# Performance work log

Hardware: AMD Instinct MI355X
Metric: run time of the kernel (lower is better)

## Reference

```python
import jax, jax.numpy as jnp
import numpy as np

K = 3          # kernel size
PAD = 1        # padding
# deformable conv v2: offset conv (2*K*K ch), modulator conv (K*K ch, 2*sigmoid), main 3x3 conv, ReLU


def _conv2d(x, w, b):
    y = jax.lax.conv_general_dilated(x, w, (1, 1), ((PAD, PAD), (PAD, PAD)),
                                     dimension_numbers=('NCHW', 'OIHW', 'NCHW'))
    return y + b[None, :, None, None]


def _bilinear_gather(x, py, px):
    # x: [B,C,H,W]; py/px: [B,K2,H,W] float sample coords; zero outside image.
    B, C, H, W = x.shape
    y0 = jnp.floor(py)
    x0 = jnp.floor(px)
    wy1 = py - y0
    wx1 = px - x0
    wy0 = 1.0 - wy1
    wx0 = 1.0 - wx1
    xf = x.reshape(B, C, H * W)

    def gather(yi, xi):
        valid = (yi >= 0) & (yi <= H - 1) & (xi >= 0) & (xi <= W - 1)
        yc = jnp.clip(yi, 0, H - 1).astype(jnp.int32)
        xc = jnp.clip(xi, 0, W - 1).astype(jnp.int32)
        idx = (yc * W + xc).reshape(B, -1)                      # [B, K2*H*W]
        v = jax.vmap(lambda xb, ib: xb[:, ib])(xf, idx)         # [B, C, K2*H*W]
        v = v.reshape(B, C, *yi.shape[1:])                      # [B, C, K2, H, W]
        return v * valid[:, None].astype(x.dtype)

    return (gather(y0, x0) * (wy0 * wx0)[:, None]
            + gather(y0, x0 + 1) * (wy0 * wx1)[:, None]
            + gather(y0 + 1, x0) * (wy1 * wx0)[:, None]
            + gather(y0 + 1, x0 + 1) * (wy1 * wx1)[:, None])


def _deform_conv(data, w, b, w_off, b_off, w_mod, b_mod):
    B, Cin, H, W = data.shape
    off = _conv2d(data, w_off, b_off)                           # [B, 2*K2, H, W]
    mask = 2.0 * jax.nn.sigmoid(_conv2d(data, w_mod, b_mod))    # [B, K2, H, W]
    off = off.reshape(B, K * K, 2, H, W)                        # (dy, dx) per tap
    dy, dx = off[:, :, 0], off[:, :, 1]
    ki, kj = jnp.meshgrid(jnp.arange(K), jnp.arange(K), indexing='ij')
    ki = ki.reshape(-1).astype(data.dtype)
    kj = kj.reshape(-1).astype(data.dtype)
    hs = jnp.arange(H, dtype=data.dtype)
    ws = jnp.arange(W, dtype=data.dtype)
    py = hs[None, None, :, None] - PAD + ki[None, :, None, None] + dy
    px = ws[None, None, None, :] - PAD + kj[None, :, None, None] + dx
    sampled = _bilinear_gather(data, py, px)                    # [B, Cin, K2, H, W]
    sampled = sampled * mask[:, None]
    out = jnp.einsum('bckhw,ock->bohw', sampled, w.reshape(w.shape[0], Cin, K * K))
    return out + b[None, :, None, None]


def setup_inputs() -> dict:
    key = jax.random.key(0)
    ks = jax.random.split(key, 7)
    B, Cin, Cout, H, W = 8, 64, 64, 128, 128
    fan = Cin * K * K
    return {
        'data': jax.random.normal(ks[0], (B, Cin, H, W), jnp.float32),
        'w': jax.random.normal(ks[1], (Cout, Cin, K, K), jnp.float32) / np.sqrt(fan),
        'b': jax.random.normal(ks[2], (Cout,), jnp.float32) * 0.01,
        'w_off': jax.random.normal(ks[3], (2 * K * K, Cin, K, K), jnp.float32) * (0.1 / np.sqrt(fan)),
        'b_off': jnp.zeros((2 * K * K,), jnp.float32),
        'w_mod': jax.random.normal(ks[4], (K * K, Cin, K, K), jnp.float32) * (0.1 / np.sqrt(fan)),
        'b_mod': jnp.zeros((K * K,), jnp.float32),
    }


def reference(data, w, b, w_off, b_off, w_mod, b_mod):
    return jax.nn.relu(_deform_conv(data, w, b, w_off, b_off, w_mod, b_mod))
```

## Files before the change

kernel.cpp:

```cpp
#include <hip/hip_runtime.h>
#include <hip/hip_fp16.h>
#include <cstdint>


typedef _Float16 half8 __attribute__((ext_vector_type(8)));
typedef __attribute__((ext_vector_type(4))) float floatx4;

__device__ __forceinline__ unsigned int pack2h(float lo, float hi) {
    __half2 h = __floats2half2_rn(lo, hi);
    union { __half2 h; unsigned int u; } cv; cv.h = h;
    return cv.u;
}
__device__ __forceinline__ unsigned int blend2h(unsigned int a, unsigned int b,
                                                unsigned int c, unsigned int d,
                                                const __half2* w) {
    union { unsigned int u; __half2 h; } A, B, C, D, O;
    A.u = a; B.u = b; C.u = c; D.u = d;
    __half2 s = __hmul2(A.h, w[0]);
    s = __hfma2(B.h, w[1], s);
    s = __hfma2(C.h, w[2], s);
    s = __hfma2(D.h, w[3], s);
    O.h = s;
    return O.u;
}

#define OFF_DATAT 0u
#define OFF_OFFP  16777216u
#define OFF_WM    30932992u
#define OFF_W27   31006720u
#define OFF_B27   31043584u

__global__ __launch_bounds__(256) void prep_k(const float* __restrict__ x,
                                              unsigned short* __restrict__ xt,
                                              const float* __restrict__ w,
                                              const float* __restrict__ w_off,
                                              const float* __restrict__ w_mod,
                                              const float* __restrict__ b_off,
                                              const float* __restrict__ b_mod,
                                              unsigned short* __restrict__ wpackM,
                                              unsigned short* __restrict__ wq,
                                              float* __restrict__ bias27) {
    __shared__ float tile[64][65];
    int blk = blockIdx.x;
    if (blk < 2048) {
        int b    = blk >> 8;
        int pos0 = (blk & 255) << 6;
        int lane = threadIdx.x & 63;
        int g    = threadIdx.x >> 6;
        for (int c = g; c < 64; c += 4)
            tile[c][lane] = x[(((b << 6) + c) << 14) + pos0 + lane];
        __syncthreads();
        int c2 = lane & 31;
        for (int i = g; i < 32; i += 4) {
            int pr = (i << 1) + (lane >> 5);
            unsigned int d = pack2h(tile[c2 << 1][pr], tile[(c2 << 1) + 1][pr]);
            *(unsigned int*)&xt[((size_t)((b << 14) + pos0 + pr) << 6) + (c2 << 1)] = d;
        }
        return;
    }
    int t = (blk - 2048) * 256 + threadIdx.x;
    if (t < 64 * 576) {
        int o = t / 576, kk = t % 576;
        int k = kk >> 6, c = kk & 63;
        wpackM[t] = __half_as_ushort(__float2half_rn(w[(o * 64 + c) * 9 + k]));
        return;
    }
    t -= 64 * 576;
    if (t < 32 * 576) {
        int o = t / 576, kk = t % 576;
        int k = kk >> 6, c = kk & 63;
        float v = 0.f;
        if (o < 18)      v = w_off[(o * 64 + c) * 9 + k];
        else if (o < 27) v = w_mod[((o - 18) * 64 + c) * 9 + k];
        int s = o >> 4, r = o & 15;
        int chh = c >> 5, q = (c >> 3) & 3, j = c & 7;
        int dst = (((((k << 1) + chh) << 1) + s) << 9) + (q << 7) + (r << 3) + j;
        wq[dst] = __half_as_ushort(__float2half_rn(v));
        if (kk == 0) bias27[o] = (o < 18) ? b_off[o] : (o < 27 ? b_mod[o - 18] : 0.f);
    }
}

__global__ __launch_bounds__(256) void conv27_k(const unsigned short* __restrict__ xt,
                                                const unsigned short* __restrict__ wq,
                                                const float* __restrict__ bias27,
                                                float* __restrict__ offP) {
    int blk   = blockIdx.x;
    int b     = blk >> 7;
    int patch = blk & 127;
    int m     = patch >> 1;
    int h     = patch & 1;
    int tid   = threadIdx.x;
    int lane  = tid & 63, wv = tid >> 6;
    int r = lane & 15, q = lane >> 4;

    const unsigned short* xb = xt + ((size_t)b << 20);
    int rb  = (m << 1) - 1;
    int cxb = (h << 6) + (wv << 4) + r - 1;
    int chq = (q << 3);

    floatx4 acc[4] = {};
    #pragma unroll
    for (int k = 0; k < 9; ++k) {
        int ki = k / 3, kj = k % 3;
        #pragma unroll
        for (int chh = 0; chh < 2; ++chh) {
            int abase = ((((k << 1) + chh) << 1) << 9) + (lane << 3);
            half8 a0 = *(const half8*)&wq[abase];
            half8 a1 = *(const half8*)&wq[abase + 512];
            #pragma unroll
            for (int tr = 0; tr < 2; ++tr) {
                int sy = rb + tr + ki;
                int sx = cxb + kj;
                half8 bf = {};
                if ((unsigned)sy < 128u && (unsigned)sx < 128u)
                    bf = *(const half8*)&xb[(size_t)(((sy << 7) + sx) << 6) + (chh << 5) + chq];
                acc[0 + tr] = __builtin_amdgcn_mfma_f32_16x16x32_f16(a0, bf, acc[0 + tr], 0, 0, 0);
                acc[2 + tr] = __builtin_amdgcn_mfma_f32_16x16x32_f16(a1, bf, acc[2 + tr], 0, 0, 0);
            }
        }
    }

    #pragma unroll
    for (int s = 0; s < 2; ++s) {
        #pragma unroll
        for (int tr = 0; tr < 2; ++tr) {
            #pragma unroll
            for (int reg = 0; reg < 4; ++reg) {
                int oc = (s << 4) + (q << 2) + reg;
                if (oc >= 27) continue;
                int pos = (((m << 1) + tr) << 7) + (h << 6) + (wv << 4) + r;
                float v = acc[(s << 1) + tr][reg] + bias27[oc];
                int kk, comp;
                if (oc < 18) { kk = oc >> 1; comp = oc & 1; }
                else         { kk = oc - 18; comp = 2; v = 2.f / (1.f + __expf(-v)); }
                offP[(size_t)(((b * 9 + kk) * 3 + comp) << 14) + pos] = v;
            }
        }
    }
}

__global__ __launch_bounds__(256, 3) void deform_main_k(const unsigned short* __restrict__ xt,
                                                        const unsigned short* __restrict__ wpackM,
                                                        const float* __restrict__ offP,
                                                        const float* __restrict__ bias,
                                                        float* __restrict__ out) {
    __shared__ ushort4 pOff[576];
    __shared__ uint4   pW[576];
    __shared__ unsigned short samp[2][64][72];
    int blk  = blockIdx.x;
    int b    = blk >> 8;
    int pos0 = (blk & 255) << 6;
    int tid  = threadIdx.x;
    int lane = tid & 63, wv = tid >> 6;
    int r = lane & 15, q = lane >> 4;
    int pg = lane >> 3;
    int j8 = lane & 7;

    const char* xbb = (const char*)(xt + ((size_t)b << 20));

    for (int e = tid; e < 576; e += 256) {
        int k = e >> 6, p = e & 63;
        int pos = pos0 + p;
        const float* offk = offP + ((size_t)((b * 9 + k) * 3) << 14);
        float dy = offk[pos];
        float dx = offk[16384 + pos];
        float m  = offk[32768 + pos];
        float py = (float)(pos >> 7) + (float)(k / 3 - 1) + dy;
        float px = (float)(pos & 127) + (float)(k % 3 - 1) + dx;
        float y0f = floorf(py), x0f = floorf(px);
        int y0 = (int)y0f, x0 = (int)x0f;
        float wy1 = py - y0f, wx1 = px - x0f;
        float wy0 = 1.f - wy1, wx0 = 1.f - wx1;
        bool vy0 = (y0 >= 0) && (y0 < 128);
        bool vy1 = (y0 >= -1) && (y0 < 127);
        bool vx0 = (x0 >= 0) && (x0 < 128);
        bool vx1 = (x0 >= -1) && (x0 < 127);
        float w00 = (vy0 && vx0) ? m * wy0 * wx0 : 0.f;
        float w01 = (vy0 && vx1) ? m * wy0 * wx1 : 0.f;
        float w10 = (vy1 && vx0) ? m * wy1 * wx0 : 0.f;
        float w11 = (vy1 && vx1) ? m * wy1 * wx1 : 0.f;
        int y0c = min(max(y0, 0), 127), y1c = min(max(y0 + 1, 0), 127);
        int x0c = min(max(x0, 0), 127), x1c = min(max(x0 + 1, 0), 127);
        ushort4 io;
        io.x = (unsigned short)((y0c << 7) + x0c);
        io.y = (unsigned short)((y0c << 7) + x1c);
        io.z = (unsigned short)((y1c << 7) + x0c);
        io.w = (unsigned short)((y1c << 7) + x1c);
        pOff[e] = io;
        union { uint4 u; __half2 h[4]; } pw;
        pw.h[0] = __float2half2_rn(w00);
        pw.h[1] = __float2half2_rn(w01);
        pw.h[2] = __float2half2_rn(w10);
        pw.h[3] = __float2half2_rn(w11);
        pW[e] = pw.u;
    }
    __syncthreads();

    floatx4 acc[4] = {};
    const char* xp = xbb + (j8 << 4);
    const unsigned short* wrow = wpackM + ((wv << 4) + r) * 576 + (q << 3);

    uint4   c00[2][2], c01[2][2], c10[2][2], c11[2][2];
    uint4   cwS[2][2];
    ushort4 nio[2];
    uint4   ncw[2];
    half8   afC[2], afN[2];

    auto readParams = [&](int k) {
        #pragma unroll
        for (int i = 0; i < 2; ++i) {
            int e  = (k << 6) + (wv << 4) + (i << 3) + pg;
            nio[i] = pOff[e];
            ncw[i] = pW[e];
        }
    };
    auto issueInto = [&](int s) {
        #pragma unroll
        for (int i = 0; i < 2; ++i) {
            cwS[s][i] = ncw[i];
            c00[s][i] = *(const uint4*)(xp + ((int)nio[i].x << 7));
            c01[s][i] = *(const uint4*)(xp + ((int)nio[i].y << 7));
            c10[s][i] = *(const uint4*)(xp + ((int)nio[i].z << 7));
            c11[s][i] = *(const uint4*)(xp + ((int)nio[i].w << 7));
        }
    };
    auto blendStore = [&](int s, int buf) {
        #pragma unroll
        for (int i = 0; i < 2; ++i) {
            int p = (wv << 4) + (i << 3) + pg;
            union { uint4 u; __half2 h[4]; } W; W.u = cwS[s][i];
            uint4 o4;
            o4.x = blend2h(c00[s][i].x, c01[s][i].x, c10[s][i].x, c11[s][i].x, W.h);
            o4.y = blend2h(c00[s][i].y, c01[s][i].y, c10[s][i].y, c11[s][i].y, W.h);
            o4.z = blend2h(c00[s][i].z, c01[s][i].z, c10[s][i].z, c11[s][i].z, W.h);
            o4.w = blend2h(c00[s][i].w, c01[s][i].w, c10[s][i].w, c11[s][i].w, W.h);
            *(uint4*)&samp[buf][p][j8 << 3] = o4;
        }
    };

    auto ldsBarrier = [&]() {
        asm volatile("s_waitcnt lgkmcnt(0)\n\ts_barrier" ::: "memory");
    };

    readParams(0); issueInto(0);
    readParams(1); issueInto(1);
    afC[0] = *(const half8*)&wrow[0];
    afC[1] = *(const half8*)&wrow[32];
    blendStore(0, 0);
    readParams(2);

    #pragma unroll
    for (int k = 0; k < 9; ++k) {
        if (k <= 6) issueInto(k & 1);
        if (k < 8) {
            afN[0] = *(const half8*)&wrow[((k + 1) << 6)];
            afN[1] = *(const half8*)&wrow[((k + 1) << 6) + 32];
        }
        ldsBarrier();
        #pragma unroll
        for (int ch = 0; ch < 2; ++ch) {
            #pragma unroll
            for (int nt = 0; nt < 4; ++nt) {
                half8 bfrag = *(const half8*)&samp[k & 1][(nt << 4) + r][(ch << 5) + (q << 3)];
                acc[nt] = __builtin_amdgcn_mfma_f32_16x16x32_f16(afC[ch], bfrag, acc[nt], 0, 0, 0);
            }
        }
        if (k < 8) {
            blendStore((k + 1) & 1, (k + 1) & 1);
            if (k <= 5) readParams(k + 3);
            afC[0] = afN[0];
            afC[1] = afN[1];
        }
    }

    #pragma unroll
    for (int nt = 0; nt < 4; ++nt) {
        #pragma unroll
        for (int reg = 0; reg < 4; ++reg) {
            int oc  = (wv << 4) + (q << 2) + reg;
            int pos = pos0 + (nt << 4) + r;
            float v = acc[nt][reg] + bias[oc];
            out[(size_t)(((b << 6) + oc) << 14) + pos] = fmaxf(v, 0.f);
        }
    }
}

extern "C" void kernel_launch(void* const* d_in, const int* in_sizes, int n_in,
                              void* d_out, int out_size, void* d_ws, size_t ws_size,
                              hipStream_t stream) {
    const float* data  = (const float*)d_in[0];
    const float* w     = (const float*)d_in[1];
    const float* bias  = (const float*)d_in[2];
    const float* w_off = (const float*)d_in[3];
    const float* b_off = (const float*)d_in[4];
    const float* w_mod = (const float*)d_in[5];
    const float* b_mod = (const float*)d_in[6];
    float* out = (float*)d_out;

    char* ws = (char*)d_ws;
    unsigned short* dataT   = (unsigned short*)(ws + OFF_DATAT);
    float*          offP    = (float*)(ws + OFF_OFFP);
    unsigned short* wpackM  = (unsigned short*)(ws + OFF_WM);
    unsigned short* wq      = (unsigned short*)(ws + OFF_W27);
    float*          bias27  = (float*)(ws + OFF_B27);

    prep_k<<<2264, 256, 0, stream>>>(data, dataT, w, w_off, w_mod,
                                     b_off, b_mod, wpackM, wq, bias27);
    conv27_k<<<1024, 256, 0, stream>>>(dataT, wq, bias27, offP);
    deform_main_k<<<2048, 256, 0, stream>>>(dataT, wpackM, offP, bias, out);
}
```

Measured before the change: 160.7 us.

## Fuse three kernels into one cooperative persistent kernel with grid syncs

```diff
diff --git a/kernel.cpp b/kernel.cpp
--- a/kernel.cpp
+++ b/kernel.cpp
@@ -1,6 +1,9 @@
 #include <hip/hip_runtime.h>
 #include <hip/hip_fp16.h>
+#include <hip/hip_cooperative_groups.h>
 #include <cstdint>
+
+namespace cg = cooperative_groups;
 
 
 typedef _Float16 half8 __attribute__((ext_vector_type(8)));
@@ -30,257 +33,260 @@
 #define OFF_W27   31006720u
 #define OFF_B27   31043584u
 
-__global__ __launch_bounds__(256) void prep_k(const float* __restrict__ x,
-                                              unsigned short* __restrict__ xt,
-                                              const float* __restrict__ w,
-                                              const float* __restrict__ w_off,
-                                              const float* __restrict__ w_mod,
-                                              const float* __restrict__ b_off,
-                                              const float* __restrict__ b_mod,
-                                              unsigned short* __restrict__ wpackM,
-                                              unsigned short* __restrict__ wq,
-                                              float* __restrict__ bias27) {
-    __shared__ float tile[64][65];
-    int blk = blockIdx.x;
-    if (blk < 2048) {
-        int b    = blk >> 8;
-        int pos0 = (blk & 255) << 6;
-        int lane = threadIdx.x & 63;
-        int g    = threadIdx.x >> 6;
-        for (int c = g; c < 64; c += 4)
-            tile[c][lane] = x[(((b << 6) + c) << 14) + pos0 + lane];
-        __syncthreads();
-        int c2 = lane & 31;
-        for (int i = g; i < 32; i += 4) {
-            int pr = (i << 1) + (lane >> 5);
-            unsigned int d = pack2h(tile[c2 << 1][pr], tile[(c2 << 1) + 1][pr]);
-            *(unsigned int*)&xt[((size_t)((b << 14) + pos0 + pr) << 6) + (c2 << 1)] = d;
-        }
-        return;
-    }
-    int t = (blk - 2048) * 256 + threadIdx.x;
-    if (t < 64 * 576) {
-        int o = t / 576, kk = t % 576;
-        int k = kk >> 6, c = kk & 63;
-        wpackM[t] = __half_as_ushort(__float2half_rn(w[(o * 64 + c) * 9 + k]));
-        return;
-    }
-    t -= 64 * 576;
-    if (t < 32 * 576) {
-        int o = t / 576, kk = t % 576;
-        int k = kk >> 6, c = kk & 63;
-        float v = 0.f;
-        if (o < 18)      v = w_off[(o * 64 + c) * 9 + k];
-        else if (o < 27) v = w_mod[((o - 18) * 64 + c) * 9 + k];
-        int s = o >> 4, r = o & 15;
-        int chh = c >> 5, q = (c >> 3) & 3, j = c & 7;
-        int dst = (((((k << 1) + chh) << 1) + s) << 9) + (q << 7) + (r << 3) + j;
-        wq[dst] = __half_as_ushort(__float2half_rn(v));
-        if (kk == 0) bias27[o] = (o < 18) ? b_off[o] : (o < 27 ? b_mod[o - 18] : 0.f);
-    }
-}
-
-__global__ __launch_bounds__(256) void conv27_k(const unsigned short* __restrict__ xt,
-                                                const unsigned short* __restrict__ wq,
-                                                const float* __restrict__ bias27,
-                                                float* __restrict__ offP) {
-    int blk   = blockIdx.x;
-    int b     = blk >> 7;
-    int patch = blk & 127;
-    int m     = patch >> 1;
-    int h     = patch & 1;
-    int tid   = threadIdx.x;
-    int lane  = tid & 63, wv = tid >> 6;
-    int r = lane & 15, q = lane >> 4;
-
-    const unsigned short* xb = xt + ((size_t)b << 20);
-    int rb  = (m << 1) - 1;
-    int cxb = (h << 6) + (wv << 4) + r - 1;
-    int chq = (q << 3);
-
-    floatx4 acc[4] = {};
-    #pragma unroll
-    for (int k = 0; k < 9; ++k) {
-        int ki = k / 3, kj = k % 3;
-        #pragma unroll
-        for (int chh = 0; chh < 2; ++chh) {
-            int abase = ((((k << 1) + chh) << 1) << 9) + (lane << 3);
-            half8 a0 = *(const half8*)&wq[abase];
-            half8 a1 = *(const half8*)&wq[abase + 512];
-            #pragma unroll
-            for (int tr = 0; tr < 2; ++tr) {
-                int sy = rb + tr + ki;
-                int sx = cxb + kj;
-                half8 bf = {};
-                if ((unsigned)sy < 128u && (unsigned)sx < 128u)
-                    bf = *(const half8*)&xb[(size_t)(((sy << 7) + sx) << 6) + (chh << 5) + chq];
-                acc[0 + tr] = __builtin_amdgcn_mfma_f32_16x16x32_f16(a0, bf, acc[0 + tr], 0, 0, 0);
-                acc[2 + tr] = __builtin_amdgcn_mfma_f32_16x16x32_f16(a1, bf, acc[2 + tr], 0, 0, 0);
-            }
-        }
-    }
-
-    #pragma unroll
-    for (int s = 0; s < 2; ++s) {
-        #pragma unroll
-        for (int tr = 0; tr < 2; ++tr) {
-            #pragma unroll
-            for (int reg = 0; reg < 4; ++reg) {
-                int oc = (s << 4) + (q << 2) + reg;
-                if (oc >= 27) continue;
-                int pos = (((m << 1) + tr) << 7) + (h << 6) + (wv << 4) + r;
-                float v = acc[(s << 1) + tr][reg] + bias27[oc];
-                int kk, comp;
-                if (oc < 18) { kk = oc >> 1; comp = oc & 1; }
-                else         { kk = oc - 18; comp = 2; v = 2.f / (1.f + __expf(-v)); }
-                offP[(size_t)(((b * 9 + kk) * 3 + comp) << 14) + pos] = v;
-            }
-        }
-    }
-}
-
-__global__ __launch_bounds__(256, 3) void deform_main_k(const unsigned short* __restrict__ xt,
-                                                        const unsigned short* __restrict__ wpackM,
-                                                        const float* __restrict__ offP,
-                                                        const float* __restrict__ bias,
-                                                        float* __restrict__ out) {
-    __shared__ ushort4 pOff[576];
-    __shared__ uint4   pW[576];
-    __shared__ unsigned short samp[2][64][72];
-    int blk  = blockIdx.x;
-    int b    = blk >> 8;
-    int pos0 = (blk & 255) << 6;
+__global__ __launch_bounds__(256, 4) void mega_k(const float* __restrict__ x,
+                                                 unsigned short* __restrict__ xt,
+                                                 const float* __restrict__ w,
+                                                 const float* __restrict__ w_off,
+                                                 const float* __restrict__ w_mod,
+                                                 const float* __restrict__ b_off,
+                                                 const float* __restrict__ b_mod,
+                                                 unsigned short* __restrict__ wpackM,
+                                                 unsigned short* __restrict__ wq,
+                                                 float* __restrict__ bias27,
+                                                 float* __restrict__ offP,
+                                                 const float* __restrict__ bias,
+                                                 float* __restrict__ out) {
+    __shared__ __align__(16) char smem[32256];
+    cg::grid_group grid = cg::this_grid();
+
     int tid  = threadIdx.x;
     int lane = tid & 63, wv = tid >> 6;
     int r = lane & 15, q = lane >> 4;
-    int pg = lane >> 3;
-    int j8 = lane & 7;
-
-    const char* xbb = (const char*)(xt + ((size_t)b << 20));
-
-    for (int e = tid; e < 576; e += 256) {
-        int k = e >> 6, p = e & 63;
-        int pos = pos0 + p;
-        const float* offk = offP + ((size_t)((b * 9 + k) * 3) << 14);
-        float dy = offk[pos];
-        float dx = offk[16384 + pos];
-        float m  = offk[32768 + pos];
-        float py = (float)(pos >> 7) + (float)(k / 3 - 1) + dy;
-        float px = (float)(pos & 127) + (float)(k % 3 - 1) + dx;
-        float y0f = floorf(py), x0f = floorf(px);
-        int y0 = (int)y0f, x0 = (int)x0f;
-        float wy1 = py - y0f, wx1 = px - x0f;
-        float wy0 = 1.f - wy1, wx0 = 1.f - wx1;
-        bool vy0 = (y0 >= 0) && (y0 < 128);
-        bool vy1 = (y0 >= -1) && (y0 < 127);
-        bool vx0 = (x0 >= 0) && (x0 < 128);
-        bool vx1 = (x0 >= -1) && (x0 < 127);
-        float w00 = (vy0 && vx0) ? m * wy0 * wx0 : 0.f;
-        float w01 = (vy0 && vx1) ? m * wy0 * wx1 : 0.f;
-        float w10 = (vy1 && vx0) ? m * wy1 * wx0 : 0.f;
-        float w11 = (vy1 && vx1) ? m * wy1 * wx1 : 0.f;
-        int y0c = min(max(y0, 0), 127), y1c = min(max(y0 + 1, 0), 127);
-        int x0c = min(max(x0, 0), 127), x1c = min(max(x0 + 1, 0), 127);
-        ushort4 io;
-        io.x = (unsigned short)((y0c << 7) + x0c);
-        io.y = (unsigned short)((y0c << 7) + x1c);
-        io.z = (unsigned short)((y1c << 7) + x0c);
-        io.w = (unsigned short)((y1c << 7) + x1c);
-        pOff[e] = io;
-        union { uint4 u; __half2 h[4]; } pw;
-        pw.h[0] = __float2half2_rn(w00);
-        pw.h[1] = __float2half2_rn(w01);
-        pw.h[2] = __float2half2_rn(w10);
-        pw.h[3] = __float2half2_rn(w11);
-        pW[e] = pw.u;
+
+    {
+        float (*tile)[65] = (float (*)[65])smem;
+        for (int blk = blockIdx.x; blk < 2264; blk += gridDim.x) {
+            if (blk < 2048) {
+                int b    = blk >> 8;
+                int pos0 = (blk & 255) << 6;
+                int g    = tid >> 6;
+                for (int c = g; c < 64; c += 4)
+                    tile[c][lane] = x[(((b << 6) + c) << 14) + pos0 + lane];
+                __syncthreads();
+                int c2 = lane & 31;
+                for (int i = g; i < 32; i += 4) {
+                    int pr = (i << 1) + (lane >> 5);
+                    unsigned int d = pack2h(tile[c2 << 1][pr], tile[(c2 << 1) + 1][pr]);
+                    *(unsigned int*)&xt[((size_t)((b << 14) + pos0 + pr) << 6) + (c2 << 1)] = d;
+                }
+                __syncthreads();
+            } else {
+                int t = (blk - 2048) * 256 + tid;
+                if (t < 64 * 576) {
+                    int o = t / 576, kk = t % 576;
+                    int k = kk >> 6, c = kk & 63;
+                    wpackM[t] = __half_as_ushort(__float2half_rn(w[(o * 64 + c) * 9 + k]));
+                } else {
+                    t -= 64 * 576;
+                    if (t < 32 * 576) {
+                        int o = t / 576, kk = t % 576;
+                        int k = kk >> 6, c = kk & 63;
+                        float v = 0.f;
+                        if (o < 18)      v = w_off[(o * 64 + c) * 9 + k];
+                        else if (o < 27) v = w_mod[((o - 18) * 64 + c) * 9 + k];
+                        int s = o >> 4, rr = o & 15;
+                        int chh = c >> 5, qq = (c >> 3) & 3, j = c & 7;
+                        int dst = (((((k << 1) + chh) << 1) + s) << 9) + (qq << 7) + (rr << 3) + j;
+                        wq[dst] = __half_as_ushort(__float2half_rn(v));
+                        if (kk == 0) bias27[o] = (o < 18) ? b_off[o] : (o < 27 ? b_mod[o - 18] : 0.f);
+                    }
+                }
+            }
+        }
     }
-    __syncthreads();
-
-    floatx4 acc[4] = {};
-    const char* xp = xbb + (j8 << 4);
-    const unsigned short* wrow = wpackM + ((wv << 4) + r) * 576 + (q << 3);
-
-    uint4   c00[2][2], c01[2][2], c10[2][2], c11[2][2];
-    uint4   cwS[2][2];
-    ushort4 nio[2];
-    uint4   ncw[2];
-    half8   afC[2], afN[2];
-
-    auto readParams = [&](int k) {
+    __threadfence();
+    grid.sync();
+
+    for (int blk = blockIdx.x; blk < 1024; blk += gridDim.x) {
+        int b     = blk >> 7;
+        int patch = blk & 127;
+        int m     = patch >> 1;
+        int h     = patch & 1;
+
+        const unsigned short* xb = xt + ((size_t)b << 20);
+        int rb  = (m << 1) - 1;
+        int cxb = (h << 6) + (wv << 4) + r - 1;
+        int chq = (q << 3);
+
+        floatx4 acc[4] = {};
         #pragma unroll
-        for (int i = 0; i < 2; ++i) {
-            int e  = (k << 6) + (wv << 4) + (i << 3) + pg;
-            nio[i] = pOff[e];
-            ncw[i] = pW[e];
+        for (int k = 0; k < 9; ++k) {
+            int ki = k / 3, kj = k % 3;
+            #pragma unroll
+            for (int chh = 0; chh < 2; ++chh) {
+                int abase = ((((k << 1) + chh) << 1) << 9) + (lane << 3);
+                half8 a0 = *(const half8*)&wq[abase];
+                half8 a1 = *(const half8*)&wq[abase + 512];
+                #pragma unroll
+                for (int tr = 0; tr < 2; ++tr) {
+                    int sy = rb + tr + ki;
+                    int sx = cxb + kj;
+                    half8 bf = {};
+                    if ((unsigned)sy < 128u && (unsigned)sx < 128u)
+                        bf = *(const half8*)&xb[(size_t)(((sy << 7) + sx) << 6) + (chh << 5) + chq];
+                    acc[0 + tr] = __builtin_amdgcn_mfma_f32_16x16x32_f16(a0, bf, acc[0 + tr], 0, 0, 0);
+                    acc[2 + tr] = __builtin_amdgcn_mfma_f32_16x16x32_f16(a1, bf, acc[2 + tr], 0, 0, 0);
+                }
+            }
         }
-    };
-    auto issueInto = [&](int s) {
+
         #pragma unroll
-        for (int i = 0; i < 2; ++i) {
-            cwS[s][i] = ncw[i];
-            c00[s][i] = *(const uint4*)(xp + ((int)nio[i].x << 7));
-            c01[s][i] = *(const uint4*)(xp + ((int)nio[i].y << 7));
-            c10[s][i] = *(const uint4*)(xp + ((int)nio[i].z << 7));
-            c11[s][i] = *(const uint4*)(xp + ((int)nio[i].w << 7));
+        for (int s = 0; s < 2; ++s) {
+            #pragma unroll
+            for (int tr = 0; tr < 2; ++tr) {
+                #pragma unroll
+                for (int reg = 0; reg < 4; ++reg) {
+                    int oc = (s << 4) + (q << 2) + reg;
+                    if (oc >= 27) continue;
+                    int pos = (((m << 1) + tr) << 7) + (h << 6) + (wv << 4) + r;
+                    float v = acc[(s << 1) + tr][reg] + bias27[oc];
+                    int kk, comp;
+                    if (oc < 18) { kk = oc >> 1; comp = oc & 1; }
+                    else         { kk = oc - 18; comp = 2; v = 2.f / (1.f + __expf(-v)); }
+                    offP[(size_t)(((b * 9 + kk) * 3 + comp) << 14) + pos] = v;
+                }
+            }
         }
-    };
-    auto blendStore = [&](int s, int buf) {
-        #pragma unroll
-        for (int i = 0; i < 2; ++i) {
-            int p = (wv << 4) + (i << 3) + pg;
-            union { uint4 u; __half2 h[4]; } W; W.u = cwS[s][i];
-            uint4 o4;
-            o4.x = blend2h(c00[s][i].x, c01[s][i].x, c10[s][i].x, c11[s][i].x, W.h);
-            o4.y = blend2h(c00[s][i].y, c01[s][i].y, c10[s][i].y, c11[s][i].y, W.h);
-            o4.z = blend2h(c00[s][i].z, c01[s][i].z, c10[s][i].z, c11[s][i].z, W.h);
-            o4.w = blend2h(c00[s][i].w, c01[s][i].w, c10[s][i].w, c11[s][i].w, W.h);
-            *(uint4*)&samp[buf][p][j8 << 3] = o4;
-        }
-    };
-
-    auto ldsBarrier = [&]() {
-        asm volatile("s_waitcnt lgkmcnt(0)\n\ts_barrier" ::: "memory");
-    };
-
-    readParams(0); issueInto(0);
-    readParams(1); issueInto(1);
-    afC[0] = *(const half8*)&wrow[0];
-    afC[1] = *(const half8*)&wrow[32];
-    blendStore(0, 0);
-    readParams(2);
-
-    #pragma unroll
-    for (int k = 0; k < 9; ++k) {
-        if (k <= 6) issueInto(k & 1);
-        if (k < 8) {
-            afN[0] = *(const half8*)&wrow[((k + 1) << 6)];
-            afN[1] = *(const half8*)&wrow[((k + 1) << 6) + 32];
-        }
-        ldsBarrier();
-        #pragma unroll
-        for (int ch = 0; ch < 2; ++ch) {
+    }
+    __threadfence();
+    grid.sync();
+
+    {
+        ushort4* pOff = (ushort4*)smem;
+        uint4*   pW   = (uint4*)(smem + 4608);
+        unsigned short (*samp)[64][72] = (unsigned short (*)[64][72])(smem + 13824);
+        int pg = lane >> 3;
+        int j8 = lane & 7;
+
+        for (int tb = blockIdx.x; tb < 2048; tb += gridDim.x) {
+            int b    = tb >> 8;
+            int pos0 = (tb & 255) << 6;
+            const char* xbb = (const char*)(xt + ((size_t)b << 20));
+
+            for (int e = tid; e < 576; e += 256) {
+                int k = e >> 6, p = e & 63;
+                int pos = pos0 + p;
+                const float* offk = offP + ((size_t)((b * 9 + k) * 3) << 14);
+                float dy = offk[pos];
+                float dx = offk[16384 + pos];
+                float m  = offk[32768 + pos];
+                float py = (float)(pos >> 7) + (float)(k / 3 - 1) + dy;
+                float px = (float)(pos & 127) + (float)(k % 3 - 1) + dx;
+                float y0f = floorf(py), x0f = floorf(px);
+                int y0 = (int)y0f, x0 = (int)x0f;
+                float wy1 = py - y0f, wx1 = px - x0f;
+                float wy0 = 1.f - wy1, wx0 = 1.f - wx1;
+                bool vy0 = (y0 >= 0) && (y0 < 128);
+                bool vy1 = (y0 >= -1) && (y0 < 127);
+                bool vx0 = (x0 >= 0) && (x0 < 128);
+                bool vx1 = (x0 >= -1) && (x0 < 127);
+                float w00 = (vy0 && vx0) ? m * wy0 * wx0 : 0.f;
+                float w01 = (vy0 && vx1) ? m * wy0 * wx1 : 0.f;
+                float w10 = (vy1 && vx0) ? m * wy1 * wx0 : 0.f;
+                float w11 = (vy1 && vx1) ? m * wy1 * wx1 : 0.f;
+                int y0c = min(max(y0, 0), 127), y1c = min(max(y0 + 1, 0), 127);
+                int x0c = min(max(x0, 0), 127), x1c = min(max(x0 + 1, 0), 127);
+                ushort4 io;
+                io.x = (unsigned short)((y0c << 7) + x0c);
+                io.y = (unsigned short)((y0c << 7) + x1c);
+                io.z = (unsigned short)((y1c << 7) + x0c);
+                io.w = (unsigned short)((y1c << 7) + x1c);
+                pOff[e] = io;
+                union { uint4 u; __half2 h[4]; } pw;
+                pw.h[0] = __float2half2_rn(w00);
+                pw.h[1] = __float2half2_rn(w01);
+                pw.h[2] = __float2half2_rn(w10);
+                pw.h[3] = __float2half2_rn(w11);
+                pW[e] = pw.u;
+            }
+            __syncthreads();
+
+            floatx4 acc[4] = {};
+            const char* xp = xbb + (j8 << 4);
+            const unsigned short* wrow = wpackM + ((wv << 4) + r) * 576 + (q << 3);
+
+            uint4   c00[2][2], c01[2][2], c10[2][2], c11[2][2];
+            uint4   cwS[2][2];
+            ushort4 nio[2];
+            uint4   ncw[2];
+            half8   afC[2], afN[2];
+
+            auto readParams = [&](int k) {
+                #pragma unroll
+                for (int i = 0; i < 2; ++i) {
+                    int e  = (k << 6) + (wv << 4) + (i << 3) + pg;
+                    nio[i] = pOff[e];
+                    ncw[i] = pW[e];
+                }
+            };
+            auto issueInto = [&](int s) {
+                #pragma unroll
+                for (int i = 0; i < 2; ++i) {
+                    cwS[s][i] = ncw[i];
+                    c00[s][i] = *(const uint4*)(xp + ((int)nio[i].x << 7));
+                    c01[s][i] = *(const uint4*)(xp + ((int)nio[i].y << 7));
+                    c10[s][i] = *(const uint4*)(xp + ((int)nio[i].z << 7));
+                    c11[s][i] = *(const uint4*)(xp + ((int)nio[i].w << 7));
+                }
+            };
+            auto blendStore = [&](int s, int buf) {
+                #pragma unroll
+                for (int i = 0; i < 2; ++i) {
+                    int p = (wv << 4) + (i << 3) + pg;
+                    union { uint4 u; __half2 h[4]; } W; W.u = cwS[s][i];
+                    uint4 o4;
+                    o4.x = blend2h(c00[s][i].x, c01[s][i].x, c10[s][i].x, c11[s][i].x, W.h);
+                    o4.y = blend2h(c00[s][i].y, c01[s][i].y, c10[s][i].y, c11[s][i].y, W.h);
+                    o4.z = blend2h(c00[s][i].z, c01[s][i].z, c10[s][i].z, c11[s][i].z, W.h);
+                    o4.w = blend2h(c00[s][i].w, c01[s][i].w, c10[s][i].w, c11[s][i].w, W.h);
+                    *(uint4*)&samp[buf][p][j8 << 3] = o4;
+                }
+            };
+            auto ldsBarrier = [&]() {
+                asm volatile("s_waitcnt lgkmcnt(0)\n\ts_barrier" ::: "memory");
+            };
+
+            readParams(0); issueInto(0);
+            readParams(1); issueInto(1);
+            afC[0] = *(const half8*)&wrow[0];
+            afC[1] = *(const half8*)&wrow[32];
+            blendStore(0, 0);
+            readParams(2);
+
+            #pragma unroll
+            for (int k = 0; k < 9; ++k) {
+                if (k <= 6) issueInto(k & 1);
+                if (k < 8) {
+                    afN[0] = *(const half8*)&wrow[((k + 1) << 6)];
+                    afN[1] = *(const half8*)&wrow[((k + 1) << 6) + 32];
+                }
+                ldsBarrier();
+                #pragma unroll
+                for (int ch = 0; ch < 2; ++ch) {
+                    #pragma unroll
+                    for (int nt = 0; nt < 4; ++nt) {
+                        half8 bfrag = *(const half8*)&samp[k & 1][(nt << 4) + r][(ch << 5) + (q << 3)];
+                        acc[nt] = __builtin_amdgcn_mfma_f32_16x16x32_f16(afC[ch], bfrag, acc[nt], 0, 0, 0);
+                    }
+                }
+                if (k < 8) {
+                    blendStore((k + 1) & 1, (k + 1) & 1);
+                    if (k <= 5) readParams(k + 3);
+                    afC[0] = afN[0];
+                    afC[1] = afN[1];
+                }
+            }
+
             #pragma unroll
             for (int nt = 0; nt < 4; ++nt) {
-                half8 bfrag = *(const half8*)&samp[k & 1][(nt << 4) + r][(ch << 5) + (q << 3)];
-                acc[nt] = __builtin_amdgcn_mfma_f32_16x16x32_f16(afC[ch], bfrag, acc[nt], 0, 0, 0);
-            }
-        }
-        if (k < 8) {
-            blendStore((k + 1) & 1, (k + 1) & 1);
-            if (k <= 5) readParams(k + 3);
-            afC[0] = afN[0];
-            afC[1] = afN[1];
-        }
-    }
-
-    #pragma unroll
-    for (int nt = 0; nt < 4; ++nt) {
-        #pragma unroll
-        for (int reg = 0; reg < 4; ++reg) {
-            int oc  = (wv << 4) + (q << 2) + reg;
-            int pos = pos0 + (nt << 4) + r;
-            float v = acc[nt][reg] + bias[oc];
-            out[(size_t)(((b << 6) + oc) << 14) + pos] = fmaxf(v, 0.f);
+                #pragma unroll
+                for (int reg = 0; reg < 4; ++reg) {
+                    int oc  = (wv << 4) + (q << 2) + reg;
+                    int pos = pos0 + (nt << 4) + r;
+                    float v = acc[nt][reg] + bias[oc];
+                    out[(size_t)(((b << 6) + oc) << 14) + pos] = fmaxf(v, 0.f);
+                }
+            }
         }
     }
 }
@@ -304,8 +310,20 @@
     unsigned short* wq      = (unsigned short*)(ws + OFF_W27);
     float*          bias27  = (float*)(ws + OFF_B27);
 
-    prep_k<<<2264, 256, 0, stream>>>(data, dataT, w, w_off, w_mod,
-                                     b_off, b_mod, wpackM, wq, bias27);
-    conv27_k<<<1024, 256, 0, stream>>>(dataT, wq, bias27, offP);
-    deform_main_k<<<2048, 256, 0, stream>>>(dataT, wpackM, offP, bias, out);
+    static int s_grid = 0;
+    if (s_grid == 0) {
+        int nb = 0;
+        if (hipOccupancyMaxActiveBlocksPerMultiprocessor(&nb, (const void*)mega_k,
+                                                         256, 0) != hipSuccess || nb <= 0)
+            nb = 4;
+        long g = (long)nb * 256;
+        s_grid = (int)(g < 1024 ? g : 1024);
+    }
+
+    void* args[] = { (void*)&data, (void*)&dataT, (void*)&w, (void*)&w_off,
+                     (void*)&w_mod, (void*)&b_off, (void*)&b_mod, (void*)&wpackM,
+                     (void*)&wq, (void*)&bias27, (void*)&offP, (void*)&bias,
+                     (void*)&out };
+    hipLaunchCooperativeKernel((const void*)mega_k, dim3(s_grid), dim3(256),
+                               args, 0, stream);
 }
```

New measurement: 433.2 us. 170% more time.
